# Performance work log

Hardware: AMD Instinct MI355X
Metric: run time of the kernel (lower is better)

## Reference

```python
import jax, jax.numpy as jnp
import numpy as np

D = 2048
H = 16
KV = 4
DH = D // H  # 128
REP = H // KV
ROPE_BASE = 10000.0


def _rope(x, pos):
    # x: (B, h, L, Dh), pos: (L,)
    half = x.shape[-1] // 2
    inv_freq = 1.0 / (ROPE_BASE ** (jnp.arange(0, half, dtype=jnp.float32) / half))
    ang = pos.astype(jnp.float32)[:, None] * inv_freq[None, :]          # (L, half)
    cos = jnp.concatenate([jnp.cos(ang), jnp.cos(ang)], axis=-1)        # (L, Dh)
    sin = jnp.concatenate([jnp.sin(ang), jnp.sin(ang)], axis=-1)
    x1, x2 = x[..., :half], x[..., half:]
    rot = jnp.concatenate([-x2, x1], axis=-1)
    return x * cos[None, None] + rot * sin[None, None]


def setup_inputs() -> dict:
    key = jax.random.key(0)
    ks = jax.random.split(key, 5)
    s = 1.0 / np.sqrt(D)
    return {
        "x": jax.random.normal(ks[0], (2, 2048, D), dtype=jnp.float32),
        "wq": jax.random.uniform(ks[1], (H * DH, D), jnp.float32, -s, s),
        "wk": jax.random.uniform(ks[2], (KV * DH, D), jnp.float32, -s, s),
        "wv": jax.random.uniform(ks[3], (KV * DH, D), jnp.float32, -s, s),
        "wo": jax.random.uniform(ks[4], (D, H * DH), jnp.float32, -s, s),
    }


def reference(x, wq, wk, wv, wo):
    B, T, _ = x.shape
    q = (x @ wq.T).reshape(B, T, H, DH).transpose(0, 2, 1, 3)    # (B,H,T,Dh)
    k = (x @ wk.T).reshape(B, T, KV, DH).transpose(0, 2, 1, 3)   # (B,KV,T,Dh)
    v = (x @ wv.T).reshape(B, T, KV, DH).transpose(0, 2, 1, 3)
    Tc = T  # no kv cache
    pos = jnp.arange(Tc)
    q = _rope(q, pos)
    k = _rope(k, pos)
    # GQA: repeat kv heads to match query heads
    k_full = jnp.repeat(k, REP, axis=1)                          # (B,H,Tc,Dh)
    v_full = jnp.repeat(v, REP, axis=1)
    scale = 1.0 / np.sqrt(DH)
    scores = jnp.einsum('bhtd,bhsd->bhts', q, k_full) * scale    # (B,H,T,Tc)
    row = jnp.arange(T)[:, None]
    col = jnp.arange(Tc)[None, :]
    causal = col <= row + (Tc - T)
    scores = jnp.where(causal[None, None], scores, -jnp.inf)
    attn = jax.nn.softmax(scores, axis=-1)
    out = jnp.einsum('bhts,bhsd->bhtd', attn, v_full)            # (B,H,T,Dh)
    out = out.transpose(0, 2, 1, 3).reshape(B, T, H * DH)
    return out @ wo.T
```

## Files before the change

### kernel.cpp

```cpp
#include <hip/hip_runtime.h>

typedef float f32x4 __attribute__((ext_vector_type(4)));
typedef short s16x8 __attribute__((ext_vector_type(8)));
typedef unsigned short u16;

__device__ __forceinline__ u16 f2bf(float f) {
    union { float f; unsigned u; } v; v.f = f;
    return (u16)((v.u + 0x7fffu + ((v.u >> 16) & 1u)) >> 16);
}
__device__ __forceinline__ float bf2f(u16 h) {
    union { unsigned u; float f; } v; v.u = ((unsigned)h) << 16;
    return v.f;
}
__device__ __forceinline__ float fast_exp2(float x) {
#if __has_builtin(__builtin_amdgcn_exp2f)
    return __builtin_amdgcn_exp2f(x);
#else
    return exp2f(x);
#endif
}

__device__ __forceinline__ void gload_lds16(const void* g, void* l) {
    __builtin_amdgcn_global_load_lds((__attribute__((address_space(1))) void*)g,
                                     (__attribute__((address_space(3))) void*)l, 16, 0, 0);
}

__global__ __launch_bounds__(256) void cvt_all(const float* __restrict__ x,  const float* __restrict__ wq,
                                               const float* __restrict__ wk, const float* __restrict__ wv,
                                               u16* __restrict__ xb, u16* __restrict__ wqkvb) {
    int u = blockIdx.x * 256 + threadIdx.x;
    const float* src;
    u16* dst;
    if (u < 1048576) { src = x + (size_t)u * 8; dst = xb + (size_t)u * 8; }
    else {
        int w = u - 1048576;
        dst = wqkvb + (size_t)w * 8;
        if (w < 524288)      src = wq + (size_t)w * 8;
        else if (w < 655360) src = wk + (size_t)(w - 524288) * 8;
        else                 src = wv + (size_t)(w - 655360) * 8;
    }
    const float4* p = (const float4*)src;
    float4 a = p[0], b = p[1];
    s16x8 o;
    o[0] = f2bf(a.x); o[1] = f2bf(a.y); o[2] = f2bf(a.z); o[3] = f2bf(a.w);
    o[4] = f2bf(b.x); o[5] = f2bf(b.y); o[6] = f2bf(b.z); o[7] = f2bf(b.w);
    *(s16x8*)dst = o;
}

__global__ __launch_bounds__(256) void cvt_kernel(const float* __restrict__ in,
                                                  u16* __restrict__ out, int n8) {
    int i = blockIdx.x * 256 + threadIdx.x;
    if (i >= n8) return;
    const float4* p = (const float4*)(in + (size_t)i * 8);
    float4 a = p[0], b = p[1];
    s16x8 o;
    o[0] = f2bf(a.x); o[1] = f2bf(a.y); o[2] = f2bf(a.z); o[3] = f2bf(a.w);
    o[4] = f2bf(b.x); o[5] = f2bf(b.y); o[6] = f2bf(b.z); o[7] = f2bf(b.w);
    *(s16x8*)(out + (size_t)i * 8) = o;
}

__global__ __launch_bounds__(256) void zero_acc(float* __restrict__ p, int n4) {
    int i = blockIdx.x * 256 + threadIdx.x;
    if (i >= n4) return;
    float4 z = {0.f, 0.f, 0.f, 0.f};
    ((float4*)p)[i] = z;
}

__global__ __launch_bounds__(256) void norm_split(const float* __restrict__ Oacc,
                                                  const float* __restrict__ Lacc,
                                                  u16* __restrict__ ab) {
    int i = blockIdx.x * 256 + threadIdx.x;
    int rowi = i >> 8;
    int col0 = (i & 255) * 8;
    const float* po = Oacc + ((size_t)rowi << 11) + col0;
    float Lv = Lacc[rowi * 16 + (col0 >> 7)];
    float inv = 1.0f / Lv;
    int b = rowi >> 10, tokp = rowi & 1023;
    u16* pd = ab + ((size_t)(b * 2048 + 1024 + tokp) << 11) + col0;
    float4 a = ((const float4*)po)[0], c = ((const float4*)po)[1];
    s16x8 o;
    o[0] = f2bf(a.x * inv); o[1] = f2bf(a.y * inv); o[2] = f2bf(a.z * inv); o[3] = f2bf(a.w * inv);
    o[4] = f2bf(c.x * inv); o[5] = f2bf(c.y * inv); o[6] = f2bf(c.z * inv); o[7] = f2bf(c.w * inv);
    *(s16x8*)pd = o;
}

template<int OUT>
__global__ __launch_bounds__(256) void gemm128(const u16* __restrict__ A, const u16* __restrict__ B,
                                               void* __restrict__ C, void* __restrict__ Ck,
                                               void* __restrict__ Cv, int M, int N, int K) {
    __shared__ __align__(16) u16 Ald[128 * 64];
    __shared__ __align__(16) u16 Bld[128 * 64];
    const int t = threadIdx.x, wid = t >> 6, lane = t & 63;
    const int m0 = blockIdx.y * 128, n0 = blockIdx.x * 128;
    const int ml = lane & 15, quad = lane >> 4, m7 = ml & 7;
    const int wm = (wid & 1) * 64, wn = (wid >> 1) * 64;
    const int sr = lane >> 3, sc = lane & 7;

    f32x4 acc[4][4] = {};

    for (int k0 = 0; k0 < K; k0 += 64) {
        if (k0) __syncthreads();
        #pragma unroll
        for (int i = 0; i < 4; ++i) {
            int seg = wid * 4 + i;
            int r = seg * 8 + sr;
            int c = (sc ^ (r & 7)) * 8;
            gload_lds16(A + (size_t)(m0 + r) * K + k0 + c, &Ald[seg * 512]);
            gload_lds16(B + (size_t)(n0 + r) * K + k0 + c, &Bld[seg * 512]);
        }
        __syncthreads();
        #pragma unroll
        for (int kk = 0; kk < 64; kk += 32) {
            s16x8 af[4], bf[4];
            #pragma unroll
            for (int mi = 0; mi < 4; ++mi)
                af[mi] = *(const s16x8*)&Ald[(wm + mi * 16 + ml) * 64 + (((kk >> 3) + quad) ^ m7) * 8];
            #pragma unroll
            for (int ni = 0; ni < 4; ++ni)
                bf[ni] = *(const s16x8*)&Bld[(wn + ni * 16 + ml) * 64 + (((kk >> 3) + quad) ^ m7) * 8];
            #pragma unroll
            for (int mi = 0; mi < 4; ++mi)
                #pragma unroll
                for (int ni = 0; ni < 4; ++ni)
                    acc[mi][ni] = __builtin_amdgcn_mfma_f32_16x16x32_bf16(af[mi], bf[ni], acc[mi][ni], 0, 0, 0);
        }
    }
    #pragma unroll
    for (int mi = 0; mi < 4; ++mi)
        #pragma unroll
        for (int ni = 0; ni < 4; ++ni) {
            int gmb = m0 + wm + mi * 16 + quad * 4;
            int gn  = n0 + wn + ni * 16 + ml;
            if constexpr (OUT == 4) {
                if (n0 < 2048) {
                    #pragma unroll
                    for (int r = 0; r < 4; ++r)
                        ((u16*)C)[(size_t)(gmb + r) * 2048 + gn] = f2bf(acc[mi][ni][r]);
                } else if (n0 < 2560) {
                    #pragma unroll
                    for (int r = 0; r < 4; ++r)
                        ((u16*)Ck)[(size_t)(gmb + r) * 512 + (gn - 2048)] = f2bf(acc[mi][ni][r]);
                } else {
                    ushort4 v;
                    v.x = f2bf(acc[mi][ni][0]); v.y = f2bf(acc[mi][ni][1]);
                    v.z = f2bf(acc[mi][ni][2]); v.w = f2bf(acc[mi][ni][3]);
                    *(ushort4*)((u16*)Cv + (size_t)(gn - 2560) * M + gmb) = v;
                }
            } else {
                #pragma unroll
                for (int r = 0; r < 4; ++r)
                    ((float*)C)[(size_t)(gmb + r) * N + gn] = acc[mi][ni][r];
            }
        }
}

__global__ __launch_bounds__(256) void rope_kernel(u16* __restrict__ qb, u16* __restrict__ kb,
                                                   int nq, int ntot, float sq) {
    int idx = blockIdx.x * 256 + threadIdx.x;
    if (idx >= ntot) return;
    u16* base; int nheads; float scl; int id;
    if (idx < nq) { base = qb; nheads = 16; scl = sq;  id = idx; }
    else          { base = kb; nheads = 4;  scl = 1.f; id = idx - nq; }
    int i = id & 63;
    int rest = id >> 6;
    int hh = rest % nheads;
    int tok = rest / nheads;
    int tpos = tok & 2047;
    u16* row = base + (size_t)tok * nheads * 128 + hh * 128;
    float x1 = bf2f(row[i]);
    float x2 = bf2f(row[i + 64]);
    float inv = expf(-(float)i * 0.14391156731570787f);
    float ang = (float)tpos * inv;
    float s, c;
    sincosf(ang, &s, &c);
    row[i]      = f2bf((x1 * c - x2 * s) * scl);
    row[i + 64] = f2bf((x2 * c + x1 * s) * scl);
}

__global__ __launch_bounds__(256, 4) void attn_kernel(const u16* __restrict__ Q, const u16* __restrict__ Kb,
                                                      const u16* __restrict__ Vt, u16* __restrict__ O) {
    __shared__ __align__(16) u16 Klds[64 * 128];
    __shared__ __align__(16) u16 Vlds[128 * 64];
    __shared__ __align__(16) u16 Plds[4][16 * 64];
    const int t = threadIdx.x, wslot = t >> 6, lane = t & 63;
    const int kv = blockIdx.y, b = blockIdx.z;
    const int g = kv + 4 * b;
    const int bx = blockIdx.x;
    int qt;
    switch ((g >> 1) & 3) {
        case 0:  qt = bx; break;
        case 1:  qt = 127 - bx; break;
        case 2:  qt = (bx + 64) & 127; break;
        default: qt = (63 - bx) & 127; break;
    }
    const int h = kv * 4 + wslot;
    const int ml = lane & 15, quad = lane >> 4, m7 = ml & 7;
    const int t0 = qt * 16;
    const int n = (qt >> 2) + 1;

    s16x8 qf[4];
    {
        const u16* qp = Q + ((size_t)(b * 2048 + t0 + ml) * 2048 + h * 128);
        #pragma unroll
        for (int kc = 0; kc < 4; ++kc)
            qf[kc] = *(const s16x8*)(qp + kc * 32 + quad * 8);
    }

    s16x8 ones;
    #pragma unroll
    for (int j = 0; j < 8; ++j) ones[j] = (short)0x3F80;

    f32x4 Oa[8] = {};
    f32x4 L = {};

    for (int it = 0; it < n; ++it) {
        const int s0 = it * 64;
        if (it) __syncthreads();
        #pragma unroll
        for (int i = 0; i < 4; ++i) {
            int seg = wslot * 4 + i;
            int kr = seg * 4 + (lane >> 4);
            int kc = ((lane & 15) ^ (kr & 7)) * 8;
            gload_lds16(Kb + (size_t)(b * 2048 + s0 + kr) * 512 + kv * 128 + kc, &Klds[seg * 512]);
            int vr = seg * 8 + (lane >> 3);
            int vc = ((lane & 7) ^ (vr & 7)) * 8;
            gload_lds16(Vt + (size_t)(kv * 128 + vr) * 4096 + b * 2048 + s0 + vc, &Vlds[seg * 512]);
        }
        __syncthreads();

        f32x4 S[4] = {};
        #pragma unroll
        for (int kc = 0; kc < 4; ++kc)
            #pragma unroll
            for (int ti = 0; ti < 4; ++ti) {
                s16x8 kf = *(const s16x8*)&Klds[(ti * 16 + ml) * 128 + ((kc * 4 + quad) ^ m7) * 8];
                S[ti] = __builtin_amdgcn_mfma_f32_16x16x32_bf16(qf[kc], kf, S[ti], 0, 0, 0);
            }

        {
            u16* pl = &Plds[wslot][0];
            const bool diag = (it == n - 1);
            #pragma unroll
            for (int r = 0; r < 4; ++r) {
                int qr = t0 + quad * 4 + r;
                int row = quad * 4 + r;
                #pragma unroll
                for (int ti = 0; ti < 4; ++ti) {
                    float e = fast_exp2(S[ti][r]);
                    if (diag && (s0 + ti * 16 + ml > qr)) e = 0.f;
                    union { float f; unsigned u; } cv; cv.f = e;
                    pl[row * 64 + (((ti * 2 + (ml >> 3)) ^ (row & 7)) * 8) + (ml & 7)] = (u16)(cv.u >> 16);
                }
            }
        }
        asm volatile("s_waitcnt lgkmcnt(0)" ::: "memory");
        s16x8 pf[2];
        pf[0] = *(const s16x8*)&Plds[wslot][ml * 64 + ((quad)     ^ m7) * 8];
        pf[1] = *(const s16x8*)&Plds[wslot][ml * 64 + ((4 + quad) ^ m7) * 8];
        asm volatile("s_waitcnt lgkmcnt(0)" ::: "memory");

        #pragma unroll
        for (int c = 0; c < 2; ++c) {
            #pragma unroll
            for (int nt = 0; nt < 8; ++nt) {
                s16x8 vf = *(const s16x8*)&Vlds[(nt * 16 + ml) * 64 + ((c * 4 + quad) ^ m7) * 8];
                Oa[nt] = __builtin_amdgcn_mfma_f32_16x16x32_bf16(pf[c], vf, Oa[nt], 0, 0, 0);
            }
            L = __builtin_amdgcn_mfma_f32_16x16x32_bf16(pf[c], ones, L, 0, 0, 0);
        }
    }

    #pragma unroll
    for (int nt = 0; nt < 8; ++nt)
        #pragma unroll
        for (int r = 0; r < 4; ++r) {
            int col = h * 128 + nt * 16 + ml;
            O[(size_t)(b * 2048 + t0 + quad * 4 + r) * 2048 + col] = f2bf(Oa[nt][r] / L[r]);
        }
}

__global__ __launch_bounds__(256, 4) void attn_split(const u16* __restrict__ Q, const u16* __restrict__ Kb,
                                                     const u16* __restrict__ Vt, u16* __restrict__ O,
                                                     float* __restrict__ Oacc, float* __restrict__ Lacc) {
    __shared__ __align__(16) u16 Klds[64 * 128];
    __shared__ __align__(16) u16 Vlds[128 * 64];
    __shared__ __align__(16) u16 Plds[4][16 * 64];
    const int t = threadIdx.x, wslot = t >> 6, lane = t & 63;
    const int id = blockIdx.x;
    const int g = id & 7, w = id >> 3;
    const int kv = g & 3, b = g >> 2;

    int qt, it0, it1, nfull;
    bool partial;
    if (w < 128) {
        qt = 127 - (w >> 1);
        nfull = (qt >> 2) + 1;
        int nA = nfull >> 1;
        if ((w & 1) == 0) { it0 = 0;  it1 = nA; }
        else              { it0 = nA; it1 = nfull; }
        partial = true;
    } else {
        qt = 191 - w;
        nfull = (qt >> 2) + 1;
        it0 = 0; it1 = nfull;
        partial = false;
    }

    const int h = kv * 4 + wslot;
    const int ml = lane & 15, quad = lane >> 4, m7 = ml & 7;
    const int t0 = qt * 16;

    s16x8 qf[4];
    {
        const u16* qp = Q + ((size_t)(b * 2048 + t0 + ml) * 2048 + h * 128);
        #pragma unroll
        for (int kc = 0; kc < 4; ++kc)
            qf[kc] = *(const s16x8*)(qp + kc * 32 + quad * 8);
    }

    s16x8 ones;
    #pragma unroll
    for (int j = 0; j < 8; ++j) ones[j] = (short)0x3F80;

    f32x4 Oa[8] = {};
    f32x4 L = {};

    for (int it = it0; it < it1; ++it) {
        const int s0 = it * 64;
        if (it != it0) __syncthreads();
        #pragma unroll
        for (int i = 0; i < 4; ++i) {
            int seg = wslot * 4 + i;
            int kr = seg * 4 + (lane >> 4);
            int kc = ((lane & 15) ^ (kr & 7)) * 8;
            gload_lds16(Kb + (size_t)(b * 2048 + s0 + kr) * 512 + kv * 128 + kc, &Klds[seg * 512]);
            int vr = seg * 8 + (lane >> 3);
            int vc = ((lane & 7) ^ (vr & 7)) * 8;
            gload_lds16(Vt + (size_t)(kv * 128 + vr) * 4096 + b * 2048 + s0 + vc, &Vlds[seg * 512]);
        }
        __syncthreads();

        f32x4 S[4] = {};
        #pragma unroll
        for (int kc = 0; kc < 4; ++kc)
            #pragma unroll
            for (int ti = 0; ti < 4; ++ti) {
                s16x8 kf = *(const s16x8*)&Klds[(ti * 16 + ml) * 128 + ((kc * 4 + quad) ^ m7) * 8];
                S[ti] = __builtin_amdgcn_mfma_f32_16x16x32_bf16(qf[kc], kf, S[ti], 0, 0, 0);
            }

        {
            u16* pl = &Plds[wslot][0];
            const bool diag = (it == nfull - 1);
            #pragma unroll
            for (int r = 0; r < 4; ++r) {
                int qr = t0 + quad * 4 + r;
                int row = quad * 4 + r;
                #pragma unroll
                for (int ti = 0; ti < 4; ++ti) {
                    float e = fast_exp2(S[ti][r]);
                    if (diag && (s0 + ti * 16 + ml > qr)) e = 0.f;
                    union { float f; unsigned u; } cv; cv.f = e;
                    pl[row * 64 + (((ti * 2 + (ml >> 3)) ^ (row & 7)) * 8) + (ml & 7)] = (u16)(cv.u >> 16);
                }
            }
        }
        asm volatile("s_waitcnt lgkmcnt(0)" ::: "memory");
        s16x8 pf[2];
        pf[0] = *(const s16x8*)&Plds[wslot][ml * 64 + ((quad)     ^ m7) * 8];
        pf[1] = *(const s16x8*)&Plds[wslot][ml * 64 + ((4 + quad) ^ m7) * 8];
        asm volatile("s_waitcnt lgkmcnt(0)" ::: "memory");

        #pragma unroll
        for (int c = 0; c < 2; ++c) {
            #pragma unroll
            for (int nt = 0; nt < 8; ++nt) {
                s16x8 vf = *(const s16x8*)&Vlds[(nt * 16 + ml) * 64 + ((c * 4 + quad) ^ m7) * 8];
                Oa[nt] = __builtin_amdgcn_mfma_f32_16x16x32_bf16(pf[c], vf, Oa[nt], 0, 0, 0);
            }
            L = __builtin_amdgcn_mfma_f32_16x16x32_bf16(pf[c], ones, L, 0, 0, 0);
        }
    }

    if (!partial) {
        #pragma unroll
        for (int nt = 0; nt < 8; ++nt)
            #pragma unroll
            for (int r = 0; r < 4; ++r) {
                int col = h * 128 + nt * 16 + ml;
                O[(size_t)(b * 2048 + t0 + quad * 4 + r) * 2048 + col] = f2bf(Oa[nt][r] / L[r]);
            }
    } else {
        const int tokp = (qt - 64) * 16;
        #pragma unroll
        for (int nt = 0; nt < 8; ++nt)
            #pragma unroll
            for (int r = 0; r < 4; ++r) {
                size_t row = (size_t)(b * 1024 + tokp + quad * 4 + r);
                atomicAdd(&Oacc[row * 2048 + h * 128 + nt * 16 + ml], Oa[nt][r]);
            }
        if (ml == 0) {
            #pragma unroll
            for (int r = 0; r < 4; ++r) {
                size_t row = (size_t)(b * 1024 + tokp + quad * 4 + r);
                atomicAdd(&Lacc[row * 16 + h], L[r]);
            }
        }
    }
}

extern "C" void kernel_launch(void* const* d_in, const int* in_sizes, int n_in,
                              void* d_out, int out_size, void* d_ws, size_t ws_size,
                              hipStream_t stream) {
    const float* x  = (const float*)d_in[0];
    const float* wq = (const float*)d_in[1];
    const float* wk = (const float*)d_in[2];
    const float* wv = (const float*)d_in[3];
    const float* wo = (const float*)d_in[4];
    float* out = (float*)d_out;
    char* ws = (char*)d_ws;

    const size_t MB = 1024 * 1024;
    u16* xb    = (u16*)(ws);
    u16* qb    = (u16*)(ws + 16 * MB);
    u16* kb    = (u16*)(ws + 32 * MB);
    u16* vtb   = (u16*)(ws + 36 * MB);
    u16* wqkvb = (u16*)(ws + 40 * MB);
    u16* ab    = xb;
    u16* wob   = wqkvb;

    const bool split = ws_size >= 70 * MB;

    cvt_all<<<7168, 256, 0, stream>>>(x, wq, wk, wv, xb, wqkvb);

    gemm128<4><<<dim3(24, 32), 256, 0, stream>>>(xb, wqkvb, qb, kb, vtb, 4096, 3072, 2048);

    cvt_kernel<<<2048, 256, 0, stream>>>(wo, wob, 524288);

    rope_kernel<<<20480, 256, 0, stream>>>(qb, kb, 4194304, 5242880, 0.12751743f);

    if (split) {
        float* Oacc = (float*)(ws + 52 * MB);
        float* Lacc = (float*)(ws + 68 * MB);
        zero_acc<<<4128, 256, 0, stream>>>(Oacc, 1056768);
        attn_split<<<1536, 256, 0, stream>>>(qb, kb, vtb, ab, Oacc, Lacc);
        norm_split<<<2048, 256, 0, stream>>>(Oacc, Lacc, ab);
    } else {
        attn_kernel<<<dim3(128, 4, 2), 256, 0, stream>>>(qb, kb, vtb, ab);
    }

    gemm128<1><<<dim3(16, 32), 256, 0, stream>>>(ab, wob, out, nullptr, nullptr, 4096, 2048, 2048);
}
```

Before: 342.3 us.

## Split only longest query tiles and combine partials without atomics

```diff
diff --git a/kernel.cpp b/kernel.cpp
--- a/kernel.cpp
+++ b/kernel.cpp
@@ -59,28 +59,35 @@
     *(s16x8*)(out + (size_t)i * 8) = o;
 }
 
-__global__ __launch_bounds__(256) void zero_acc(float* __restrict__ p, int n4) {
+__global__ __launch_bounds__(256) void norm_comb(const float* __restrict__ Oacc,
+                                                 const float* __restrict__ Lacc,
+                                                 u16* __restrict__ ab) {
     int i = blockIdx.x * 256 + threadIdx.x;
-    if (i >= n4) return;
-    float4 z = {0.f, 0.f, 0.f, 0.f};
-    ((float4*)p)[i] = z;
-}
-
-__global__ __launch_bounds__(256) void norm_split(const float* __restrict__ Oacc,
-                                                  const float* __restrict__ Lacc,
-                                                  u16* __restrict__ ab) {
-    int i = blockIdx.x * 256 + threadIdx.x;
-    int rowi = i >> 8;
-    int col0 = (i & 255) * 8;
-    const float* po = Oacc + ((size_t)rowi << 11) + col0;
-    float Lv = Lacc[rowi * 16 + (col0 >> 7)];
-    float inv = 1.0f / Lv;
-    int b = rowi >> 10, tokp = rowi & 1023;
-    u16* pd = ab + ((size_t)(b * 2048 + 1024 + tokp) << 11) + col0;
-    float4 a = ((const float4*)po)[0], c = ((const float4*)po)[1];
+    int g = i >> 15;
+    int rem = i & 32767;
+    int qti = rem >> 10;
+    int rem2 = rem & 1023;
+    int row = rem2 >> 6;
+    int colblk = rem2 & 63;
+    int col0 = colblk * 8;
+    int head = colblk >> 4;
+    size_t tile0 = (size_t)(g * 32 + qti);
+    size_t tile1 = (size_t)((8 + g) * 32 + qti);
+    const float* p0 = Oacc + tile0 * 8192 + row * 512 + col0;
+    const float* p1 = Oacc + tile1 * 8192 + row * 512 + col0;
+    float L0 = Lacc[(tile0 * 4 + head) * 16 + row];
+    float L1 = Lacc[(tile1 * 4 + head) * 16 + row];
+    float inv = 1.0f / (L0 + L1);
+    int b = g >> 2, kv = g & 3;
+    int token = (96 + qti) * 16 + row;
+    u16* pd = ab + ((size_t)(b * 2048 + token) << 11) + kv * 512 + col0;
+    float4 a0 = ((const float4*)p0)[0], a1 = ((const float4*)p0)[1];
+    float4 b0 = ((const float4*)p1)[0], b1 = ((const float4*)p1)[1];
     s16x8 o;
-    o[0] = f2bf(a.x * inv); o[1] = f2bf(a.y * inv); o[2] = f2bf(a.z * inv); o[3] = f2bf(a.w * inv);
-    o[4] = f2bf(c.x * inv); o[5] = f2bf(c.y * inv); o[6] = f2bf(c.z * inv); o[7] = f2bf(c.w * inv);
+    o[0] = f2bf((a0.x + b0.x) * inv); o[1] = f2bf((a0.y + b0.y) * inv);
+    o[2] = f2bf((a0.z + b0.z) * inv); o[3] = f2bf((a0.w + b0.w) * inv);
+    o[4] = f2bf((a1.x + b1.x) * inv); o[5] = f2bf((a1.y + b1.y) * inv);
+    o[6] = f2bf((a1.z + b1.z) * inv); o[7] = f2bf((a1.w + b1.w) * inv);
     *(s16x8*)pd = o;
 }
 
@@ -279,31 +286,30 @@
         }
 }
 
-__global__ __launch_bounds__(256, 4) void attn_split(const u16* __restrict__ Q, const u16* __restrict__ Kb,
+__global__ __launch_bounds__(256, 4) void attn_sched(const u16* __restrict__ Q, const u16* __restrict__ Kb,
                                                      const u16* __restrict__ Vt, u16* __restrict__ O,
                                                      float* __restrict__ Oacc, float* __restrict__ Lacc) {
     __shared__ __align__(16) u16 Klds[64 * 128];
     __shared__ __align__(16) u16 Vlds[128 * 64];
     __shared__ __align__(16) u16 Plds[4][16 * 64];
     const int t = threadIdx.x, wslot = t >> 6, lane = t & 63;
-    const int id = blockIdx.x;
-    const int g = id & 7, w = id >> 3;
+    const int bid = blockIdx.x;
+    const int idx = bid >> 3, g = bid & 7;
     const int kv = g & 3, b = g >> 2;
 
-    int qt, it0, it1, nfull;
+    int qt, it0, it1, nfull, hsel = 0;
     bool partial;
-    if (w < 128) {
-        qt = 127 - (w >> 1);
-        nfull = (qt >> 2) + 1;
-        int nA = nfull >> 1;
-        if ((w & 1) == 0) { it0 = 0;  it1 = nA; }
-        else              { it0 = nA; it1 = nfull; }
+    if (idx < 32) {
+        qt = 95 - idx; nfull = (qt >> 2) + 1; it0 = 0; it1 = nfull; partial = false;
+    } else if (idx < 96) {
+        int p = (idx - 32) >> 1; hsel = (idx - 32) & 1;
+        qt = 127 - p; nfull = (qt >> 2) + 1;
+        int nh = nfull >> 1;
+        it0 = hsel ? nh : 0;
+        it1 = hsel ? nfull : nh;
         partial = true;
     } else {
-        qt = 191 - w;
-        nfull = (qt >> 2) + 1;
-        it0 = 0; it1 = nfull;
-        partial = false;
+        qt = 159 - idx; nfull = (qt >> 2) + 1; it0 = 0; it1 = nfull; partial = false;
     }
 
     const int h = kv * 4 + wslot;
@@ -391,20 +397,18 @@
                 O[(size_t)(b * 2048 + t0 + quad * 4 + r) * 2048 + col] = f2bf(Oa[nt][r] / L[r]);
             }
     } else {
-        const int tokp = (qt - 64) * 16;
+        const int qti = qt - 96;
+        float* Ob = Oacc + (size_t)((hsel * 8 + g) * 32 + qti) * 8192;
         #pragma unroll
         for (int nt = 0; nt < 8; ++nt)
             #pragma unroll
-            for (int r = 0; r < 4; ++r) {
-                size_t row = (size_t)(b * 1024 + tokp + quad * 4 + r);
-                atomicAdd(&Oacc[row * 2048 + h * 128 + nt * 16 + ml], Oa[nt][r]);
-            }
+            for (int r = 0; r < 4; ++r)
+                Ob[(quad * 4 + r) * 512 + wslot * 128 + nt * 16 + ml] = Oa[nt][r];
         if (ml == 0) {
-            #pragma unroll
-            for (int r = 0; r < 4; ++r) {
-                size_t row = (size_t)(b * 1024 + tokp + quad * 4 + r);
-                atomicAdd(&Lacc[row * 16 + h], L[r]);
-            }
+            float* Lb = Lacc + ((size_t)((hsel * 8 + g) * 32 + qti) * 4 + wslot) * 16;
+            #pragma unroll
+            for (int r = 0; r < 4; ++r)
+                Lb[quad * 4 + r] = L[r];
         }
     }
 }
@@ -442,9 +446,8 @@
     if (split) {
         float* Oacc = (float*)(ws + 52 * MB);
         float* Lacc = (float*)(ws + 68 * MB);
-        zero_acc<<<4128, 256, 0, stream>>>(Oacc, 1056768);
-        attn_split<<<1536, 256, 0, stream>>>(qb, kb, vtb, ab, Oacc, Lacc);
-        norm_split<<<2048, 256, 0, stream>>>(Oacc, Lacc, ab);
+        attn_sched<<<1280, 256, 0, stream>>>(qb, kb, vtb, ab, Oacc, Lacc);
+        norm_comb<<<1024, 256, 0, stream>>>(Oacc, Lacc, ab);
     } else {
         attn_kernel<<<dim3(128, 4, 2), 256, 0, stream>>>(qb, kb, vtb, ab);
     }
```

After: 323.8 us. 5.4% less time.
